# Kernel tuning notes

Measured on AMD Instinct MI355X. Metric: run time of the kernel, lower is better.

## Reference

```python
import jax, jax.numpy as jnp
import numpy as np

B, L, N, M = 2, 4, 2048, 1024
K, DIV = 32, 4
S = K // DIV  # maxpool window along neighbor axis
F1 = 128      # prev features
PF = 64       # lift output point-feature dim
OUT = 256
EPS = 1e-5


def setup_inputs() -> dict:
    key = jax.random.key(0)
    ks = jax.random.split(key, 12)
    C_in = PF + F1  # 192, conv input channels
    return {
        "points": jax.random.normal(ks[0], (B, L, N, 3), jnp.float32),
        "queries": jax.random.normal(ks[1], (B, L, M, 3), jnp.float32),
        "feat_prev": jax.random.normal(ks[2], (B, L, N, F1), jnp.float32),
        # Lift params
        "bn1_g": jnp.ones((3,), jnp.float32),
        "bn1_b": jnp.zeros((3,), jnp.float32),
        "w1": jax.random.normal(ks[3], (PF // 2, 3), jnp.float32) * 0.3,
        "b1": jnp.zeros((PF // 2,), jnp.float32),
        "bn2_g": jnp.ones((PF // 2,), jnp.float32),
        "bn2_b": jnp.zeros((PF // 2,), jnp.float32),
        "w2": jax.random.normal(ks[4], (PF, PF // 2), jnp.float32) * 0.1,
        "b2": jnp.zeros((PF,), jnp.float32),
        # conv = BatchNorm3d(C_in) + Conv3d(C_in, OUT, (1,1,DIV))
        "bnc_g": jnp.ones((C_in,), jnp.float32),
        "bnc_b": jnp.zeros((C_in,), jnp.float32),
        "conv_w": jax.random.normal(ks[5], (OUT, C_in, DIV), jnp.float32) * 0.05,
        "conv_b": jnp.zeros((OUT,), jnp.float32),
    }


def _bn(x, g, b):
    """Training-mode batchnorm, channel = last axis (equivalent to the
    torch transpose(1,4)->BatchNorm3d->transpose(1,4) pattern)."""
    ax = tuple(range(x.ndim - 1))
    m = x.mean(ax)
    v = x.var(ax)  # biased variance, as torch uses for normalization
    return (x - m) * jax.lax.rsqrt(v + EPS) * g + b


_gather = jax.vmap(jax.vmap(lambda arr, idx: arr[idx]))  # over B, L


def reference(points, queries, feat_prev,
              bn1_g, bn1_b, w1, b1, bn2_g, bn2_b, w2, b2,
              bnc_g, bnc_b, conv_w, conv_b):
    # ---- KNN (cdist + topk, fully batched) ----
    pn = jnp.sum(points * points, -1)          # (B,L,N)
    qn = jnp.sum(queries * queries, -1)        # (B,L,M)
    cross = jnp.einsum('blmc,blnc->blmn', queries, points)
    d2 = qn[..., None] + pn[:, :, None, :] - 2.0 * cross  # (B,L,M,N)
    idx = jax.lax.top_k(-d2, K)[1]             # (B,L,M,K) ascending distance

    nn_pts = _gather(points, idx)              # (B,L,M,K,3)
    local = queries[:, :, :, None, :] - nn_pts # center - neighbors

    # ---- Lift MLP (with batchnorm) ----
    h = _bn(local, bn1_g, bn1_b)
    h = jax.nn.relu(jnp.einsum('blmki,oi->blmko', h, w1) + b1)
    h = _bn(h, bn2_g, bn2_b)
    h = jax.nn.relu(jnp.einsum('blmki,oi->blmko', h, w2) + b2)  # (B,L,M,K,PF)

    # ---- gather prev features, concat ----
    fp = _gather(feat_prev, idx)               # (B,L,M,K,F1)
    feat = jnp.concatenate([h, fp], axis=-1)   # (B,L,M,K,C_in)

    # ---- maxpool over neighbor shells: window S, stride S along K ----
    C = feat.shape[-1]
    fm = feat.reshape(B, L, M, DIV, S, C).max(axis=4)  # (B,L,M,DIV,C)

    # ---- BatchNorm3d(C_in) + Conv3d(C_in, OUT, (1,1,DIV)) ----
    fm = _bn(fm, bnc_g, bnc_b)
    out = jnp.einsum('blmdc,ocd->blmo', fm, conv_w) + conv_b  # (B,L,M,OUT)
    return out
```

## Files before the change

### kernel.cpp

```cpp
#include <hip/hip_runtime.h>
#include <cstdint>

#define B_    2
#define L_    4
#define N_    2048
#define M_    1024
#define K_    32
#define DIV_  4
#define S_    8
#define F1_   128
#define PF_   64
#define CIN_  192
#define OUT_  256
#define EPS_  1e-5f

#define BL_   (B_*L_)
#define BLM_  (BL_*M_)
#define NPTS_ (BLM_*K_)
#define ROWS_ (BLM_*DIV_)

#define OFF_FMH  0
#define OFF_IDX  3145728
#define OFF_LOC  3407872
#define OFF_W1F  4456448
#define OFF_B1F  4456544
#define OFF_W2F  4456576
#define OFF_B2F  4458624
#define OFF_WCB  4458688
#define OFF_BCF  4556992
#define OFF_P2   4557248
#define OFF_P3   4573632

typedef __attribute__((ext_vector_type(8))) short short8;
typedef __attribute__((ext_vector_type(4))) short short4v;
typedef __attribute__((ext_vector_type(4))) float f32x4;

__device__ __forceinline__ unsigned short f2bf(float f)
{
    unsigned u = __float_as_uint(f);
    unsigned r = (u + 0x7FFFu + ((u >> 16) & 1u)) >> 16;
    return (unsigned short)r;
}
__device__ __forceinline__ float bf2f(unsigned short h)
{
    unsigned u = ((unsigned)h) << 16;
    return __uint_as_float(u);
}

__global__ __launch_bounds__(512) void k_knn(const float* __restrict__ points,
                                             const float* __restrict__ queries,
                                             int*   __restrict__ idxbuf,
                                             float* __restrict__ local4,
                                             float* __restrict__ p1)
{
#pragma clang fp contract(off)
    __shared__ float4 pt[N_];
    __shared__ unsigned bufA[8][64];
    __shared__ unsigned bufN[8][64];
    __shared__ float  wred[8][8];

    const int t    = threadIdx.x;
    const int lane = t & 63;
    const int wv   = t >> 6;
    const int bl   = blockIdx.x >> 7;
    const int m    = ((blockIdx.x & 127) << 3) + wv;

    const float* P = points  + (size_t)bl * (N_*3);
    const float* Q = queries + (size_t)bl * (M_*3);

    for (int n = t; n < N_; n += 512) {
        float x = P[n*3], y = P[n*3+1], z = P[n*3+2];
        float pn = (x*x + y*y) + z*z;
        pt[n] = make_float4(x, y, z, pn);
    }
    __syncthreads();

    const float qx = Q[m*3], qy = Q[m*3+1], qz = Q[m*3+2];
    const float qn = (qx*qx + qy*qy) + qz*qz;
    const double qxd = (double)qx, qyd = (double)qy, qzd = (double)qz;

    auto uBkey = [&](unsigned n) -> unsigned long long {
        const float4 p4 = pt[n & 2047];
        double dx = qxd - (double)p4.x, dy = qyd - (double)p4.y, dz = qzd - (double)p4.z;
        double d2d = dx*dx + dy*dy + dz*dz;
        unsigned long long uB = (unsigned long long)__double_as_longlong(d2d);
        uB = (uB & 0x8000000000000000ULL) ? ~uB : (uB | 0x8000000000000000ULL);
        return (uB & ~2047ULL) | (unsigned long long)(n & 2047);
    };
    auto cmp_less = [&](unsigned pa, unsigned pn, unsigned ca, unsigned cn) -> bool {
        bool eq = (pa == ca);
        bool pl = eq ? (pn < cn) : (pa < ca);
        bool realtie = eq && (ca != 0xFFFFFFFFu);
        if (__ballot(realtie)) {
            unsigned long long pb = uBkey(pn);
            unsigned long long cb = uBkey(cn);
            if (realtie) pl = (pb < cb);
        }
        return pl;
    };

    unsigned Aa = 0xFFFFFFFFu;
    unsigned An = 2048u + lane;
    unsigned thrA = 0xFFFFFFFFu;
    int bufcnt = 0;

    auto flushfn = [&]() {
        unsigned sa, sn;
        if (lane < bufcnt) { sa = bufA[wv][lane]; sn = bufN[wv][lane]; }
        else               { sa = 0xFFFFFFFFu;    sn = 2048u + lane; }
        for (int k = 2; k <= 64; k <<= 1) {
            for (int j = k >> 1; j >= 1; j >>= 1) {
                unsigned pa = __shfl_xor(sa, j);
                unsigned pn = __shfl_xor(sn, j);
                bool wantMin = (((lane & k) == 0) == ((lane & j) == 0));
                bool pl = cmp_less(pa, pn, sa, sn);
                if (pl == wantMin) { sa = pa; sn = pn; }
            }
        }
        int src = (31 - lane) & 63;
        unsigned ba = __shfl(sa, src);
        unsigned bn = __shfl(sn, src);
        if (lane < 32) {
            if (cmp_less(ba, bn, Aa, An)) { Aa = ba; An = bn; }
        }
        for (int j = 16; j >= 1; j >>= 1) {
            unsigned pa = __shfl_xor(Aa, j);
            unsigned pn = __shfl_xor(An, j);
            bool wantMin = ((lane & j) == 0);
            bool pl = cmp_less(pa, pn, Aa, An);
            if (pl == wantMin) { Aa = pa; An = pn; }
        }
        bufcnt = 0;
        thrA = __shfl(Aa, 31);
    };

    float4 p4 = pt[lane];
    for (int r = 0; r < 32; ++r) {
        const int n = r*64 + lane;
        float4 p4n = p4;
        if (r < 31) p4n = pt[n + 64];
        float cross = (qx*p4.x + qy*p4.y) + qz*p4.z;
        float d2f = (qn + p4.w) - 2.0f*cross;
        unsigned uA = __float_as_uint(d2f);
        uA = (uA & 0x80000000u) ? ~uA : (uA | 0x80000000u);
        p4 = p4n;

        bool lt = (uA <= thrA);
        unsigned long long mask = __ballot(lt);
        int cnt = __builtin_popcountll(mask);
        if (cnt == 0) continue;
        if (bufcnt + cnt > 64) {
            flushfn();
            lt = (uA <= thrA);
            mask = __ballot(lt);
            cnt = __builtin_popcountll(mask);
            if (cnt == 0) continue;
        }
        int pos = bufcnt + __builtin_popcountll(mask & ((1ULL << lane) - 1ULL));
        if (lt) { bufA[wv][pos] = uA; bufN[wv][pos] = (unsigned)n; }
        bufcnt += cnt;
    }
    if (bufcnt > 0) flushfn();

    const long long base = ((long long)bl * M_ + m) * K_;
    float lx = 0.f, ly = 0.f, lz = 0.f;
    if (lane < 32) {
        const int n = (int)An;
        idxbuf[base + lane] = n;
        const float4 pp = pt[n];
        lx = qx - pp.x; ly = qy - pp.y; lz = qz - pp.z;
        *(float4*)(local4 + (base + lane)*4) = make_float4(lx, ly, lz, 0.f);
    }
    float s0 = lx, s1 = ly, s2 = lz, s3 = lx*lx, s4 = ly*ly, s5 = lz*lz;
#pragma unroll
    for (int off = 32; off; off >>= 1) {
        s0 += __shfl_xor(s0, off); s1 += __shfl_xor(s1, off); s2 += __shfl_xor(s2, off);
        s3 += __shfl_xor(s3, off); s4 += __shfl_xor(s4, off); s5 += __shfl_xor(s5, off);
    }
    if (lane == 0) {
        wred[wv][0]=s0; wred[wv][1]=s1; wred[wv][2]=s2;
        wred[wv][3]=s3; wred[wv][4]=s4; wred[wv][5]=s5;
    }
    __syncthreads();
    if (t < 6) {
        float s = 0.f;
#pragma unroll
        for (int w = 0; w < 8; ++w) s += wred[w][t];
        p1[(long long)blockIdx.x*8 + t] = s;
    }
}

__global__ __launch_bounds__(256) void k_fold1(const float* __restrict__ p1,
                        const float* __restrict__ w1, const float* __restrict__ b1,
                        const float* __restrict__ g,  const float* __restrict__ bb,
                        float* __restrict__ w1f, float* __restrict__ b1f)
{
    __shared__ float red[6][33];
    __shared__ float s1[3], t1[3];
    const int t = threadIdx.x;
    const int c = t >> 5, i = t & 31;
    if (c < 6) {
        float s = 0.f;
        for (int w = i; w < 1024; w += 32) s += p1[w*8 + c];
        red[c][i] = s;
    }
    __syncthreads();
    if (t < 3) {
        float S = 0.f, Q = 0.f;
        for (int k = 0; k < 32; ++k) { S += red[t][k]; Q += red[t+3][k]; }
        float mean = S / (float)NPTS_;
        float var  = Q / (float)NPTS_ - mean*mean;
        float r = 1.0f / sqrtf(var + EPS_);
        float sc = r * g[t];
        s1[t] = sc; t1[t] = bb[t] - mean*sc;
    }
    __syncthreads();
    if (t < 32) {
        float acc = b1[t];
        for (int i2 = 0; i2 < 3; ++i2) {
            float w = w1[t*3+i2];
            w1f[t*3+i2] = w * s1[i2];
            acc += w * t1[i2];
        }
        b1f[t] = acc;
    }
}

__global__ __launch_bounds__(256) void k_stats2(const float* __restrict__ local4,
                                                const float* __restrict__ w1f,
                                                const float* __restrict__ b1f,
                                                float* __restrict__ p2)
{
    __shared__ float4 pts[1024];
    __shared__ float  sred[4][64];
    const int t = threadIdx.x;
    const int lane = t & 63;
    const int wv   = t >> 6;
    const int base = blockIdx.x * 1024;

    for (int j = t; j < 1024; j += 256)
        pts[j] = *(const float4*)(local4 + (size_t)(base + j) * 4);

    const int ch = lane & 31;
    const float w0 = w1f[ch*3], w1v = w1f[ch*3+1], w2v = w1f[ch*3+2];
    const float bv = b1f[ch];
    __syncthreads();

    float s = 0.f, q = 0.f;
    const int pbase = wv*256 + (lane >> 5);
    for (int it = 0; it < 128; ++it) {
        float4 v = pts[pbase + it*2];
        float h = fmaxf(bv + w0*v.x + w1v*v.y + w2v*v.z, 0.f);
        s += h; q += h*h;
    }
    s += __shfl_xor(s, 32); q += __shfl_xor(q, 32);
    if (lane < 32) { sred[wv][lane] = s; sred[wv][32+lane] = q; }
    __syncthreads();
    if (t < 64)
        p2[blockIdx.x*64 + t] = sred[0][t]+sred[1][t]+sred[2][t]+sred[3][t];
}

__global__ void k_fold2(const float* __restrict__ p2,
                        const float* __restrict__ w2, const float* __restrict__ b2,
                        const float* __restrict__ g,  const float* __restrict__ bb,
                        float* __restrict__ w2f, float* __restrict__ b2f)
{
    __shared__ float s2[32], t2[32];
    int t = threadIdx.x;
    if (t < 32) {
        float S = 0, Q = 0;
        for (int b = 0; b < 256; ++b) { S += p2[b*64+t]; Q += p2[b*64+32+t]; }
        float mean = S / (float)NPTS_;
        float var  = Q / (float)NPTS_ - mean*mean;
        float r = 1.0f / sqrtf(var + EPS_);
        float sc = r * g[t];
        s2[t] = sc; t2[t] = bb[t] - mean*sc;
    }
    __syncthreads();
    float acc = b2[t];
    for (int i = 0; i < 32; ++i) {
        float w = w2[t*32+i];
        w2f[t*32+i] = w * s2[i];
        acc += w * t2[i];
    }
    b2f[t] = acc;
}

__global__ __launch_bounds__(256) void k_shell(const float* __restrict__ feat_prev,
                                               const int*   __restrict__ idxbuf,
                                               const float* __restrict__ local4,
                                               const float* __restrict__ w1f,
                                               const float* __restrict__ b1f,
                                               const float* __restrict__ w2f,
                                               const float* __restrict__ b2f,
                                               unsigned short* __restrict__ fmh)
{
    __shared__ float w1s[96], b1s[32];
    __shared__ int   idxs[K_];
    __shared__ float locs[K_][4];
    __shared__ __align__(16) float h1s[K_][36];

    const int t = threadIdx.x;
    const int lane = t & 63;
    const int wv   = t >> 6;
    const int blm = blockIdx.x;
    const long long base = (long long)blm * K_;

    if (t < 96)  w1s[t] = w1f[t];
    if (t >= 96 && t < 128) b1s[t-96] = b1f[t-96];
    if (t >= 128 && t < 160) idxs[t-128] = idxbuf[base + (t-128)];
    if (t < 128) ((float*)locs)[t] = local4[base*4 + t];
    __syncthreads();

    for (int j = t; j < 1024; j += 256) {
        int k = j >> 5, o = j & 31;
        float v = b1s[o] + w1s[o*3]*locs[k][0] + w1s[o*3+1]*locs[k][1] + w1s[o*3+2]*locs[k][2];
        h1s[k][o] = fmaxf(v, 0.f);
    }
    __syncthreads();

    {
        float w2c[32];
#pragma unroll
        for (int i = 0; i < 8; ++i) {
            float4 v = *(const float4*)(w2f + lane*32 + i*4);
            w2c[i*4]=v.x; w2c[i*4+1]=v.y; w2c[i*4+2]=v.z; w2c[i*4+3]=v.w;
        }
        const float b2v = b2f[lane];
        float mx = 0.0f;
#pragma unroll
        for (int kk = 0; kk < 8; ++kk) {
            const int k = wv*8 + kk;
            const float4* hp = (const float4*)&h1s[k][0];
            float acc = b2v;
#pragma unroll
            for (int c = 0; c < 8; ++c) {
                float4 h4 = hp[c];
                acc += h4.x*w2c[c*4+0];
                acc += h4.y*w2c[c*4+1];
                acc += h4.z*w2c[c*4+2];
                acc += h4.w*w2c[c*4+3];
            }
            mx = fmaxf(mx, fmaxf(acc, 0.f));
        }
        fmh[(size_t)blm*(DIV_*CIN_) + wv*CIN_ + lane] = f2bf(mx);
    }
    {
        const float* fp0 = feat_prev + (size_t)(blm / M_) * N_ * F1_;
#pragma unroll
        for (int ph = 0; ph < 2; ++ph) {
            int d = ph*2 + (t >> 7), c = t & 127;
            float mx = -3.4e38f;
#pragma unroll
            for (int j = 0; j < 8; ++j) {
                int n = idxs[d*8+j];
                mx = fmaxf(mx, fp0[(size_t)n*F1_ + c]);
            }
            fmh[(size_t)blm*(DIV_*CIN_) + d*CIN_ + 64 + c] = f2bf(mx);
        }
    }
}

__global__ void k_stats3(const unsigned short* __restrict__ fmh, float* __restrict__ p3)
{
    const int t = threadIdx.x;
    const int blk = blockIdx.x;
    float s = 0.f, q = 0.f;
    const size_t base = (size_t)blk * 128 * CIN_;
    for (int r = 0; r < 128; ++r) {
        float v = bf2f(fmh[base + (size_t)r*CIN_ + t]);
        s += v; q += v*v;
    }
    p3[blk*384 + t] = s;
    p3[blk*384 + 192 + t] = q;
}

__global__ __launch_bounds__(256) void k_fold3(const float* __restrict__ p3,
                                               const float* __restrict__ conv_w,
                                               const float* __restrict__ conv_b,
                                               const float* __restrict__ g,
                                               const float* __restrict__ bb,
                                               unsigned short* __restrict__ wcfb,
                                               float* __restrict__ bcf)
{
    __shared__ float sc[CIN_], tc[CIN_];
    const int t = threadIdx.x;
    if (t < CIN_) {
        float S = 0, Q = 0;
        for (int b = 0; b < 256; ++b) { S += p3[b*384+t]; Q += p3[b*384+192+t]; }
        float mean = S / (float)ROWS_;
        float var  = Q / (float)ROWS_ - mean*mean;
        float r = 1.0f / sqrtf(var + EPS_);
        float s = r * g[t];
        sc[t] = s; tc[t] = bb[t] - mean*s;
    }
    __syncthreads();
    const int lo = blockIdx.x * 3072;
    for (int j = lo + t; j < lo + 3072; j += 256) {
        int o = j / 768, k = j - o*768;
        int d = k / CIN_, c = k - d*CIN_;
        wcfb[j] = f2bf(conv_w[o*768 + c*4 + d] * sc[c]);
    }
    if (blockIdx.x == 0) {
        float acc = conv_b[t];
        for (int c = 0; c < CIN_; ++c) {
            float tcv = tc[c];
#pragma unroll
            for (int d = 0; d < 4; ++d) acc += tcv * conv_w[t*768 + c*4 + d];
        }
        bcf[t] = acc;
    }
}

__global__ __launch_bounds__(256) void k_gemm(const unsigned short* __restrict__ A,
                                              const unsigned short* __restrict__ Wb,
                                              const float* __restrict__ bias,
                                              float* __restrict__ C)
{
    __shared__ __align__(16) unsigned short As[128][72];
    __shared__ __align__(16) unsigned short Bs[64][72];
    const int t = threadIdx.x;
    const int lane = t & 63;
    const int wv = t >> 6;
    const int row0 = (blockIdx.x >> 2) * 128;
    const int col0 = (blockIdx.x & 3) * 64;
    const int wr = wv >> 1, wc = wv & 1;
    const int r16 = lane & 15, kq = lane >> 4;

    f32x4 acc[4][2];
#pragma unroll
    for (int i = 0; i < 4; ++i)
#pragma unroll
        for (int j = 0; j < 2; ++j) acc[i][j] = (f32x4){0.f,0.f,0.f,0.f};

    for (int kt = 0; kt < 12; ++kt) {
#pragma unroll
        for (int p = 0; p < 4; ++p) {
            int j = p*256 + t;
            int r = j >> 3, kc = (j & 7) * 8;
            *(short8*)&As[r][kc] = *(const short8*)(A + (size_t)(row0 + r)*768 + kt*64 + kc);
        }
#pragma unroll
        for (int p = 0; p < 2; ++p) {
            int j = p*256 + t;
            int r = j >> 3, kc = (j & 7) * 8;
            *(short8*)&Bs[r][kc] = *(const short8*)(Wb + (size_t)(col0 + r)*768 + kt*64 + kc);
        }
        __syncthreads();
#pragma unroll
        for (int ks = 0; ks < 2; ++ks) {
            short8 bf[2];
#pragma unroll
            for (int n = 0; n < 2; ++n) {
                const unsigned short* pb = &Bs[wc*32 + n*16 + r16][ks*32 + kq*4];
                short4v b0 = *(const short4v*)pb;
                short4v b1 = *(const short4v*)(pb + 16);
                bf[n][0]=b0[0]; bf[n][1]=b0[1]; bf[n][2]=b0[2]; bf[n][3]=b0[3];
                bf[n][4]=b1[0]; bf[n][5]=b1[1]; bf[n][6]=b1[2]; bf[n][7]=b1[3];
            }
#pragma unroll
            for (int mf = 0; mf < 4; ++mf) {
                const unsigned short* pa = &As[wr*64 + mf*16 + r16][ks*32 + kq*4];
                short4v a0 = *(const short4v*)pa;
                short4v a1 = *(const short4v*)(pa + 16);
                short8 af;
                af[0]=a0[0]; af[1]=a0[1]; af[2]=a0[2]; af[3]=a0[3];
                af[4]=a1[0]; af[5]=a1[1]; af[6]=a1[2]; af[7]=a1[3];
                acc[mf][0] = __builtin_amdgcn_mfma_f32_16x16x32_bf16(af, bf[0], acc[mf][0], 0, 0, 0);
                acc[mf][1] = __builtin_amdgcn_mfma_f32_16x16x32_bf16(af, bf[1], acc[mf][1], 0, 0, 0);
            }
        }
        __syncthreads();
    }

#pragma unroll
    for (int mf = 0; mf < 4; ++mf) {
#pragma unroll
        for (int n = 0; n < 2; ++n) {
            const int col = col0 + wc*32 + n*16 + r16;
            const float bv = bias[col];
#pragma unroll
            for (int i = 0; i < 4; ++i) {
                int row = row0 + wr*64 + mf*16 + kq*4 + i;
                C[(size_t)row*256 + col] = acc[mf][n][i] + bv;
            }
        }
    }
}

extern "C" void kernel_launch(void* const* d_in, const int* in_sizes, int n_in,
                              void* d_out, int out_size, void* d_ws, size_t ws_size,
                              hipStream_t stream)
{
    const float* points    = (const float*)d_in[0];
    const float* queries   = (const float*)d_in[1];
    const float* feat_prev = (const float*)d_in[2];
    const float* bn1g = (const float*)d_in[3];
    const float* bn1b = (const float*)d_in[4];
    const float* w1   = (const float*)d_in[5];
    const float* b1   = (const float*)d_in[6];
    const float* bn2g = (const float*)d_in[7];
    const float* bn2b = (const float*)d_in[8];
    const float* w2   = (const float*)d_in[9];
    const float* b2   = (const float*)d_in[10];
    const float* bncg = (const float*)d_in[11];
    const float* bncb = (const float*)d_in[12];
    const float* convw= (const float*)d_in[13];
    const float* convb= (const float*)d_in[14];

    float* ws   = (float*)d_ws;
    unsigned short* fmh = (unsigned short*)(ws + OFF_FMH);
    int*   idxb = (int*)(ws + OFF_IDX);
    float* loc4 = ws + OFF_LOC;
    float* w1f  = ws + OFF_W1F;
    float* b1f  = ws + OFF_B1F;
    float* w2f  = ws + OFF_W2F;
    float* b2f  = ws + OFF_B2F;
    unsigned short* wcfb = (unsigned short*)(ws + OFF_WCB);
    float* bcf  = ws + OFF_BCF;
    float* p1   = ws + OFF_FMH;
    float* p2   = ws + OFF_P2;
    float* p3   = ws + OFF_P3;

    k_knn   <<<1024, 512, 0, stream>>>(points, queries, idxb, loc4, p1);
    k_fold1 <<<1, 256, 0, stream>>>(p1, w1, b1, bn1g, bn1b, w1f, b1f);
    k_stats2<<<256, 256, 0, stream>>>(loc4, w1f, b1f, p2);
    k_fold2 <<<1, 64, 0, stream>>>(p2, w2, b2, bn2g, bn2b, w2f, b2f);
    k_shell <<<BLM_, 256, 0, stream>>>(feat_prev, idxb, loc4, w1f, b1f, w2f, b2f, fmh);
    k_stats3<<<256, 192, 0, stream>>>(fmh, p3);
    k_fold3 <<<64, 256, 0, stream>>>(p3, convw, convb, bncg, bncb, wcfb, bcf);
    k_gemm  <<<256, 256, 0, stream>>>(fmh, wcfb, bcf, (float*)d_out);
}
```

Measured before the change: 183.8 us.

## Fuse BN1 fold into stats2 and widen grids of stats and GEMM kernels

Merges the single-block k_fold1 into k_stats2: every block reduces the p1 partials and folds the BN1 parameters itself, and only block 0 writes w1f and b1f. k_stats2, k_stats3 and k_gemm now run with more, smaller blocks (1024, 512 and 512) so the 256 CUs get fuller occupancy, and the p2/p3 partial buffers grow to match, which moves the p3 offset. The cost is redundant p1 reduction in every block, more partials for the fold kernels to sum, and less operand reuse per GEMM tile.

```diff
diff --git a/kernel.cpp b/kernel.cpp
--- a/kernel.cpp
+++ b/kernel.cpp
@@ -29,7 +29,7 @@
 #define OFF_WCB  4458688
 #define OFF_BCF  4556992
 #define OFF_P2   4557248
-#define OFF_P3   4573632
+#define OFF_P3   4622784
 
 typedef __attribute__((ext_vector_type(8))) short short8;
 typedef __attribute__((ext_vector_type(4))) short short4v;
@@ -190,20 +190,33 @@
     }
 }
 
-__global__ __launch_bounds__(256) void k_fold1(const float* __restrict__ p1,
-                        const float* __restrict__ w1, const float* __restrict__ b1,
-                        const float* __restrict__ g,  const float* __restrict__ bb,
-                        float* __restrict__ w1f, float* __restrict__ b1f)
+__global__ __launch_bounds__(256) void k_stats2(const float* __restrict__ local4,
+                                                const float* __restrict__ p1,
+                                                const float* __restrict__ w1,
+                                                const float* __restrict__ b1,
+                                                const float* __restrict__ g1,
+                                                const float* __restrict__ bb1,
+                                                float* __restrict__ w1f,
+                                                float* __restrict__ b1f,
+                                                float* __restrict__ p2)
 {
     __shared__ float red[6][33];
-    __shared__ float s1[3], t1[3];
+    __shared__ float s1v[3], t1v[3];
+    __shared__ float4 pts[256];
+    __shared__ float  sred[4][64];
     const int t = threadIdx.x;
-    const int c = t >> 5, i = t & 31;
-    if (c < 6) {
-        float s = 0.f;
-        for (int w = i; w < 1024; w += 32) s += p1[w*8 + c];
-        red[c][i] = s;
-    }
+    const int lane = t & 63;
+    const int wv   = t >> 6;
+
+    {
+        const int c = t >> 5, i = t & 31;
+        if (c < 6) {
+            float s = 0.f;
+            for (int w = i; w < 1024; w += 32) s += p1[w*8 + c];
+            red[c][i] = s;
+        }
+    }
+    pts[t] = *(const float4*)(local4 + ((size_t)blockIdx.x*256 + t) * 4);
     __syncthreads();
     if (t < 3) {
         float S = 0.f, Q = 0.f;
@@ -211,44 +224,28 @@
         float mean = S / (float)NPTS_;
         float var  = Q / (float)NPTS_ - mean*mean;
         float r = 1.0f / sqrtf(var + EPS_);
-        float sc = r * g[t];
-        s1[t] = sc; t1[t] = bb[t] - mean*sc;
-    }
-    __syncthreads();
-    if (t < 32) {
+        float sc = r * g1[t];
+        s1v[t] = sc; t1v[t] = bb1[t] - mean*sc;
+    }
+    __syncthreads();
+    if (blockIdx.x == 0 && t < 32) {
         float acc = b1[t];
-        for (int i2 = 0; i2 < 3; ++i2) {
-            float w = w1[t*3+i2];
-            w1f[t*3+i2] = w * s1[i2];
-            acc += w * t1[i2];
+        for (int i = 0; i < 3; ++i) {
+            float w = w1[t*3+i];
+            w1f[t*3+i] = w * s1v[i];
+            acc += w * t1v[i];
         }
         b1f[t] = acc;
     }
-}
-
-__global__ __launch_bounds__(256) void k_stats2(const float* __restrict__ local4,
-                                                const float* __restrict__ w1f,
-                                                const float* __restrict__ b1f,
-                                                float* __restrict__ p2)
-{
-    __shared__ float4 pts[1024];
-    __shared__ float  sred[4][64];
-    const int t = threadIdx.x;
-    const int lane = t & 63;
-    const int wv   = t >> 6;
-    const int base = blockIdx.x * 1024;
-
-    for (int j = t; j < 1024; j += 256)
-        pts[j] = *(const float4*)(local4 + (size_t)(base + j) * 4);
 
     const int ch = lane & 31;
-    const float w0 = w1f[ch*3], w1v = w1f[ch*3+1], w2v = w1f[ch*3+2];
-    const float bv = b1f[ch];
-    __syncthreads();
+    const float wa = w1[ch*3], wb = w1[ch*3+1], wc = w1[ch*3+2];
+    const float w0 = wa*s1v[0], w1v = wb*s1v[1], w2v = wc*s1v[2];
+    const float bv = b1[ch] + wa*t1v[0] + wb*t1v[1] + wc*t1v[2];
 
     float s = 0.f, q = 0.f;
-    const int pbase = wv*256 + (lane >> 5);
-    for (int it = 0; it < 128; ++it) {
+    const int pbase = wv*64 + (lane >> 5);
+    for (int it = 0; it < 32; ++it) {
         float4 v = pts[pbase + it*2];
         float h = fmaxf(bv + w0*v.x + w1v*v.y + w2v*v.z, 0.f);
         s += h; q += h*h;
@@ -269,7 +266,7 @@
     int t = threadIdx.x;
     if (t < 32) {
         float S = 0, Q = 0;
-        for (int b = 0; b < 256; ++b) { S += p2[b*64+t]; Q += p2[b*64+32+t]; }
+        for (int b = 0; b < 1024; ++b) { S += p2[b*64+t]; Q += p2[b*64+32+t]; }
         float mean = S / (float)NPTS_;
         float var  = Q / (float)NPTS_ - mean*mean;
         float r = 1.0f / sqrtf(var + EPS_);
@@ -366,8 +363,8 @@
     const int t = threadIdx.x;
     const int blk = blockIdx.x;
     float s = 0.f, q = 0.f;
-    const size_t base = (size_t)blk * 128 * CIN_;
-    for (int r = 0; r < 128; ++r) {
+    const size_t base = (size_t)blk * 64 * CIN_;
+    for (int r = 0; r < 64; ++r) {
         float v = bf2f(fmh[base + (size_t)r*CIN_ + t]);
         s += v; q += v*v;
     }
@@ -387,7 +384,7 @@
     const int t = threadIdx.x;
     if (t < CIN_) {
         float S = 0, Q = 0;
-        for (int b = 0; b < 256; ++b) { S += p3[b*384+t]; Q += p3[b*384+192+t]; }
+        for (int b = 0; b < 512; ++b) { S += p3[b*384+t]; Q += p3[b*384+192+t]; }
         float mean = S / (float)ROWS_;
         float var  = Q / (float)ROWS_ - mean*mean;
         float r = 1.0f / sqrtf(var + EPS_);
@@ -417,25 +414,25 @@
                                               const float* __restrict__ bias,
                                               float* __restrict__ C)
 {
-    __shared__ __align__(16) unsigned short As[128][72];
+    __shared__ __align__(16) unsigned short As[64][72];
     __shared__ __align__(16) unsigned short Bs[64][72];
     const int t = threadIdx.x;
     const int lane = t & 63;
     const int wv = t >> 6;
-    const int row0 = (blockIdx.x >> 2) * 128;
+    const int row0 = (blockIdx.x >> 2) * 64;
     const int col0 = (blockIdx.x & 3) * 64;
     const int wr = wv >> 1, wc = wv & 1;
     const int r16 = lane & 15, kq = lane >> 4;
 
-    f32x4 acc[4][2];
-#pragma unroll
-    for (int i = 0; i < 4; ++i)
+    f32x4 acc[2][2];
+#pragma unroll
+    for (int i = 0; i < 2; ++i)
 #pragma unroll
         for (int j = 0; j < 2; ++j) acc[i][j] = (f32x4){0.f,0.f,0.f,0.f};
 
     for (int kt = 0; kt < 12; ++kt) {
 #pragma unroll
-        for (int p = 0; p < 4; ++p) {
+        for (int p = 0; p < 2; ++p) {
             int j = p*256 + t;
             int r = j >> 3, kc = (j & 7) * 8;
             *(short8*)&As[r][kc] = *(const short8*)(A + (size_t)(row0 + r)*768 + kt*64 + kc);
@@ -459,8 +456,8 @@
                 bf[n][4]=b1[0]; bf[n][5]=b1[1]; bf[n][6]=b1[2]; bf[n][7]=b1[3];
             }
 #pragma unroll
-            for (int mf = 0; mf < 4; ++mf) {
-                const unsigned short* pa = &As[wr*64 + mf*16 + r16][ks*32 + kq*4];
+            for (int mf = 0; mf < 2; ++mf) {
+                const unsigned short* pa = &As[wr*32 + mf*16 + r16][ks*32 + kq*4];
                 short4v a0 = *(const short4v*)pa;
                 short4v a1 = *(const short4v*)(pa + 16);
                 short8 af;
@@ -474,14 +471,14 @@
     }
 
 #pragma unroll
-    for (int mf = 0; mf < 4; ++mf) {
+    for (int mf = 0; mf < 2; ++mf) {
 #pragma unroll
         for (int n = 0; n < 2; ++n) {
             const int col = col0 + wc*32 + n*16 + r16;
             const float bv = bias[col];
 #pragma unroll
             for (int i = 0; i < 4; ++i) {
-                int row = row0 + wr*64 + mf*16 + kq*4 + i;
+                int row = row0 + wr*32 + mf*16 + kq*4 + i;
                 C[(size_t)row*256 + col] = acc[mf][n][i] + bv;
             }
         }
@@ -523,11 +520,10 @@
     float* p3   = ws + OFF_P3;
 
     k_knn   <<<1024, 512, 0, stream>>>(points, queries, idxb, loc4, p1);
-    k_fold1 <<<1, 256, 0, stream>>>(p1, w1, b1, bn1g, bn1b, w1f, b1f);
-    k_stats2<<<256, 256, 0, stream>>>(loc4, w1f, b1f, p2);
+    k_stats2<<<1024, 256, 0, stream>>>(loc4, p1, w1, b1, bn1g, bn1b, w1f, b1f, p2);
     k_fold2 <<<1, 64, 0, stream>>>(p2, w2, b2, bn2g, bn2b, w2f, b2f);
     k_shell <<<BLM_, 256, 0, stream>>>(feat_prev, idxb, loc4, w1f, b1f, w2f, b2f, fmh);
-    k_stats3<<<256, 192, 0, stream>>>(fmh, p3);
+    k_stats3<<<512, 192, 0, stream>>>(fmh, p3);
     k_fold3 <<<64, 256, 0, stream>>>(p3, convw, convb, bncg, bncb, wcfb, bcf);
-    k_gemm  <<<256, 256, 0, stream>>>(fmh, wcfb, bcf, (float*)d_out);
-}
+    k_gemm  <<<512, 256, 0, stream>>>(fmh, wcfb, bcf, (float*)d_out);
+}
```

New measurement: 207.1 us. 12.7% more time.
